# Performance work log

Measured on AMD Instinct MI355X. Metric: run time of the kernel, lower is better.

## Reference

```python
import jax, jax.numpy as jnp
import numpy as np

T = 1 << 20          # sequence length
THRESHOLD = 1e-4     # decay-reset threshold (module default)


def setup_inputs() -> dict:
    key = jax.random.key(0)
    X = jax.random.normal(key, (T,), dtype=jnp.float32)
    # stable params near module init [0.2, 0.2, 0.0, 0.0]; small w3/w4 keep the
    # quadratic recurrence bounded while exercising all terms.
    params = jnp.array([0.2, 0.2, 0.05, 0.01], dtype=jnp.float32)
    return {"X": X, "params": params}


def reference(X, params):
    dt = X.dtype
    w1 = jnp.tanh(params[0]); dtanh1 = 1.0 - w1 * w1; d2tanh1 = -2.0 * w1 * dtanh1
    w2 = jnp.tanh(params[1]); dtanh2 = 1.0 - w2 * w2; d2tanh2 = -2.0 * w2 * dtanh2
    w3, w4 = params[2], params[3]

    def step(carry, x):
        h, Jh, Hh, decay = carry  # h:(), Jh:(4,), Hh:(4,4), decay:()
        h_new = w1 * x + w2 * h + w3 * x * x + w4 * h * h
        df_dw = jnp.stack([x * dtanh1, h * dtanh2, x * x, h * h])
        df_dh = w2 + 2.0 * w4 * h
        Jh_new = df_dw + df_dh * Jh
        Hww = (jnp.zeros((4, 4), dt)
               .at[0, 0].set(x * d2tanh1)
               .at[1, 1].set(h * d2tanh2))
        g = jnp.zeros((4,), dt).at[1].set(dtanh2).at[3].set(2.0 * h)
        outer = g[:, None] * Jh[None, :]
        Hh_new = Hww + outer + outer.T + df_dh * Hh
        decay_new = decay * jnp.abs(df_dh)
        reset = decay_new < THRESHOLD
        # torch zero_() mutates storage in-place, so the appended J/H entries at a
        # reset step are also zeroed -> emit post-reset values.
        Jh_out = jnp.where(reset, jnp.zeros((4,), dt), Jh_new)
        Hh_out = jnp.where(reset, jnp.zeros((4, 4), dt), Hh_new)
        h_out = jnp.where(reset, jax.lax.stop_gradient(h_new), h_new)  # detach
        decay_out = jnp.where(reset, jnp.ones((), dt), decay_new)
        return (h_out, Jh_out, Hh_out, decay_out), (h_new, Jh_out, Hh_out)

    init = (jnp.zeros((), dt), jnp.zeros((4,), dt), jnp.zeros((4, 4), dt),
            jnp.ones((), dt))
    _, (hs, Js, Hs) = jax.lax.scan(step, init, X[:-1])
    Z = jnp.concatenate([jnp.zeros((1,), dt), hs])              # [T]
    J = jnp.concatenate([jnp.zeros((1, 4), dt), Js])            # [T, 4]
    H = jnp.concatenate([jnp.zeros((1, 4, 4), dt), Hs])         # [T, 4, 4]
    return Z, J, H
```

## Files before the change

kernel.cpp:

```cpp
#include <hip/hip_runtime.h>
#include <math.h>

#define TLEN (1 << 20)
#define SB 32
#define NSB (TLEN / SB)
#define SCB 256
#define NSCB (NSB / SCB)
#define THRESH 1e-4f
#define IDMAP 0x00FAC688u

#define WWORDS (SCB * SB + 8)
#define WPAD(i) ((i) + ((i) >> 5))
#define LDSW WPAD(WWORDS)

#pragma clang fp contract(off)


#define CHUNK55(OFS, OUTARR) {                                                 \
        const float4* xp_ = (const float4*)(X + (OFS) - 24);                   \
        float xa_[56];                                                         \
        _Pragma("unroll")                                                      \
        for (int q_ = 0; q_ < 14; ++q_) {                                      \
            float4 v_ = xp_[q_];                                               \
            xa_[4 * q_ + 0] = v_.x; xa_[4 * q_ + 1] = v_.y;                    \
            xa_[4 * q_ + 2] = v_.z; xa_[4 * q_ + 3] = v_.w;                    \
        }                                                                      \
        float h_ = 0.0f;                                                       \
        _Pragma("unroll")                                                      \
        for (int p_ = 0; p_ < 55; ++p_) {                                      \
            float x_ = xa_[p_];                                                \
            float t1_ = w1 * x_;                                               \
            float t2_ = w2 * h_;                                               \
            float s1_ = t1_ + t2_;                                             \
            float t3_ = (w3 * x_) * x_;                                        \
            float s2_ = s1_ + t3_;                                             \
            float t4_ = (w4 * h_) * h_;                                        \
            h_ = s2_ + t4_;                                                    \
            if (p_ >= 23) OUTARR[p_ - 23] = h_;                                \
        }                                                                      \
    }

__global__ void __launch_bounds__(256) k_zts(const float* __restrict__ P,
                                             const float* __restrict__ X,
                                             float* __restrict__ c,
                                             float* __restrict__ Z,
                                             unsigned int* __restrict__ L32,
                                             unsigned int* __restrict__ BT) {
#pragma clang fp contract(off)
    __shared__ float sc[4];
    __shared__ float zw[LDSW];
    __shared__ unsigned int buf[2][SCB];
    int t = threadIdx.x;
    int b = blockIdx.x;
    if (t == 0) {
        float tw1 = (float)tanh((double)P[0]);
        float tw2 = (float)tanh((double)P[1]);
        sc[0] = tw1; sc[1] = tw2; sc[2] = P[2]; sc[3] = P[3];
        if (b == 0) {
            float dt1 = 1.0f - tw1 * tw1;
            float dt2 = 1.0f - tw2 * tw2;
            c[0] = tw1; c[1] = tw2; c[2] = P[2]; c[3] = P[3];
            c[4] = dt1; c[5] = dt2;
            c[6] = (-2.0f * tw1) * dt1; c[7] = (-2.0f * tw2) * dt2;
            c[8] = 2.0f * P[3];
        }
    }
    __syncthreads();
    float w1 = sc[0], w2 = sc[1], w3 = sc[2], w4 = sc[3];
    float w42 = 2.0f * w4;
    long gi = (long)b * SCB + t;
    long o = gi * 32;
    float out[32];
    if (gi == 0) {
        float h = 0.0f;
        out[0] = 0.0f;
        for (int k = 0; k < 31; ++k) {
            float x = X[k];
            float t1 = w1 * x;
            float t2 = w2 * h;
            float s1 = t1 + t2;
            float t3 = (w3 * x) * x;
            float s2 = s1 + t3;
            float t4 = (w4 * h) * h;
            h = s2 + t4;
            out[k + 1] = h;
        }
    } else {
        CHUNK55(o, out);
    }
#pragma unroll
    for (int q = 0; q < 8; ++q)
        *(float4*)(Z + o + 4 * q) = make_float4(out[4 * q], out[4 * q + 1],
                                                out[4 * q + 2], out[4 * q + 3]);
    int rbase = t * 32 + 8;
#pragma unroll
    for (int k = 0; k < 32; ++k) zw[WPAD(rbase + k)] = out[k];
    if (t == 0 && b > 0) {
        long op = (long)b * (SCB * SB) - 32;
        float pout[32];
        CHUNK55(op, pout);
#pragma unroll
        for (int q = 0; q < 7; ++q) zw[WPAD(1 + q)] = pout[25 + q];
    }
    __syncthreads();
    unsigned int m32;
    if (gi < NSB - 1) {
        float d[8]; int last[8];
#pragma unroll
        for (int g = 0; g < 8; ++g) { d[g] = 1.0f; last[g] = -g; }
        if (gi == 0) {
#pragma unroll
            for (int g = 0; g < 8; ++g) last[g] = 0;
            for (int k = 0; k < 32; ++k) {
                float fa = fabsf(w2 + w42 * zw[WPAD(rbase + k)]);
#pragma unroll
                for (int g = 0; g < 8; ++g) {
                    d[g] = d[g] * fa;
                    if (d[g] < THRESH) { last[g] = k + 1; d[g] = 1.0f; }
                }
            }
        } else {
#pragma unroll
            for (int p = 0; p < 7; ++p) {
                float fa = fabsf(w2 + w42 * zw[WPAD(rbase + p - 7)]);
#pragma unroll
                for (int g = 7 - p; g < 8; ++g) {
                    d[g] = d[g] * fa;
                    if (d[g] < THRESH) { last[g] = p - 6; d[g] = 1.0f; }
                }
            }
            for (int k = 0; k < 32; ++k) {
                float fa = fabsf(w2 + w42 * zw[WPAD(rbase + k)]);
#pragma unroll
                for (int g = 0; g < 8; ++g) {
                    d[g] = d[g] * fa;
                    if (d[g] < THRESH) { last[g] = k + 1; d[g] = 1.0f; }
                }
            }
        }
        m32 = 0;
#pragma unroll
        for (int g = 0; g < 8; ++g) {
            int delta = 32 - last[g]; if (delta > 7) delta = 7;
            m32 |= (unsigned int)delta << (3 * g);
        }
    } else {
        m32 = IDMAP;
    }
    buf[0][t] = m32;
    __syncthreads();
    int cur = 0;
    for (int off = 1; off < SCB; off <<= 1) {
        unsigned int hi = buf[cur][t];
        unsigned int r;
        if (t >= off) {
            unsigned int lo = buf[cur][t - off];
            r = 0;
#pragma unroll
            for (int g = 0; g < 8; ++g) {
                unsigned int lg = (lo >> (3 * g)) & 7u;
                r |= ((hi >> (3 * lg)) & 7u) << (3 * g);
            }
        } else {
            r = hi;
        }
        buf[cur ^ 1][t] = r;
        __syncthreads();
        cur ^= 1;
    }
    L32[gi] = buf[cur][t];
    if (t == SCB - 1) BT[b] = buf[cur][t];
}

__global__ void __launch_bounds__(256) k_jh6(const float* __restrict__ X,
                                             const float* __restrict__ Z,
                                             const float* __restrict__ c,
                                             const unsigned int* __restrict__ L32,
                                             const unsigned int* __restrict__ BT,
                                             float* __restrict__ Jout,
                                             float* __restrict__ Hout) {
#pragma clang fp contract(off)
    __shared__ unsigned int sBT[NSCB];
    __shared__ unsigned char ages[256];
    __shared__ float zs[264];
    __shared__ float xs[264];
    __shared__ float hx[256 * 17];
    int t = threadIdx.x;
    int B = blockIdx.x;
    float w2 = c[1], dt1 = c[4], dt2 = c[5], d2t1 = c[6], d2t2 = c[7], w42 = c[8];
    long base = (long)B * 256 - 8;
    if (t < NSCB) sBT[t] = BT[t];
    if (t >= 128 && t < 194) {
        int s = t - 128;
        long zi = base + 4l * s;
        float4 v = make_float4(0.f, 0.f, 0.f, 0.f);
        if (zi >= 0) v = *(const float4*)(Z + zi);
        zs[4 * s] = v.x; zs[4 * s + 1] = v.y; zs[4 * s + 2] = v.z; zs[4 * s + 3] = v.w;
    } else if (t >= 194 && t < 260 - 0 && t < 256) {
        int s = t - 194;
        long zi = base + 4l * s;
        float4 v = make_float4(0.f, 0.f, 0.f, 0.f);
        if (zi >= 0) v = *(const float4*)(X + zi);
        xs[4 * s] = v.x; xs[4 * s + 1] = v.y; xs[4 * s + 2] = v.z; xs[4 * s + 3] = v.w;
    } else if (t >= 64 && t < 68) {
        int s = t - 64 + 62;
        long zi = base + 4l * s;
        float4 v = make_float4(0.f, 0.f, 0.f, 0.f);
        if (zi >= 0) v = *(const float4*)(X + zi);
        xs[4 * s] = v.x; xs[4 * s + 1] = v.y; xs[4 * s + 2] = v.z; xs[4 * s + 3] = v.w;
    }
    __syncthreads();
    if (t < 8) {
        int i = B * 8 + t;
        int e = 0;
        if (i > 0) {
            int bp = (i - 1) >> 8;
            unsigned int g = 0;
            for (int k = 0; k < bp; ++k) g = (sBT[k] >> (3 * g)) & 7u;
            e = (int)((L32[i - 1] >> (3 * g)) & 7u);
        }
        long ci = (long)i * SB;
        long r = ci - e;
        float d = 1.0f;
        long last = r;
        for (long m = r + 1; m <= ci; ++m) {
            float a = w2 + w42 * zs[(int)(m - 1 - base)];
            d = d * fabsf(a);
            if (d < THRESH) { last = m; d = 1.0f; }
        }
        ages[t * 32] = (unsigned char)(ci - last);
        for (int k = 1; k < SB; ++k) {
            long m = ci + k;
            float a = w2 + w42 * zs[(int)(m - 1 - base)];
            d = d * fabsf(a);
            if (d < THRESH) { last = m; d = 1.0f; }
            ages[t * 32 + k] = (unsigned char)(m - last);
        }
    }
    __syncthreads();
    long q = (long)B * 256 + t;
    int a = (int)ages[t];
    float J0 = 0, J1 = 0, J2 = 0, J3 = 0;
    float H00 = 0, H01 = 0, H03 = 0, H11 = 0, H12 = 0, H13 = 0, H23 = 0, H33 = 0;
    if (a > 0) {
        long m0 = q - a + 1;
        {
            int ix = (int)(m0 - 1 - base);
            float x = xs[ix];
            float h = zs[ix];
            H00 = x * d2t1; H11 = h * d2t2;
            J0 = x * dt1; J1 = h * dt2; J2 = x * x; J3 = h * h;
        }
        for (long m = m0 + 1; m <= q; ++m) {
            int ix = (int)(m - 1 - base);
            float x = xs[ix];
            float h = zs[ix];
            float av = w2 + w42 * h;
            float g3 = 2.0f * h;
            float g1J0 = dt2 * J0, g1J1 = dt2 * J1, g1J2 = dt2 * J2, g1J3 = dt2 * J3;
            float g3J0 = g3 * J0, g3J1 = g3 * J1, g3J2 = g3 * J2, g3J3 = g3 * J3;
            float n00 = (x * d2t1) + av * H00;
            float n01 = g1J0 + av * H01;
            float n03 = g3J0 + av * H03;
            float n11 = (((h * d2t2) + g1J1) + g1J1) + av * H11;
            float n12 = g1J2 + av * H12;
            float n13 = (g1J3 + g3J1) + av * H13;
            float n23 = g3J2 + av * H23;
            float n33 = (g3J3 + g3J3) + av * H33;
            H00 = n00; H01 = n01; H03 = n03; H11 = n11;
            H12 = n12; H13 = n13; H23 = n23; H33 = n33;
            J0 = (x * dt1) + av * J0;
            J1 = (h * dt2) + av * J1;
            J2 = (x * x) + av * J2;
            J3 = (h * h) + av * J3;
        }
    }
    *((float4*)(Jout + 4 * q)) = make_float4(J0, J1, J2, J3);
    float* hr = hx + t * 17;
    hr[0]  = H00; hr[1]  = H01; hr[2]  = 0.0f; hr[3]  = H03;
    hr[4]  = H01; hr[5]  = H11; hr[6]  = H12;  hr[7]  = H13;
    hr[8]  = 0.0f; hr[9] = H12; hr[10] = 0.0f; hr[11] = H23;
    hr[12] = H03; hr[13] = H13; hr[14] = H23;  hr[15] = H33;
    __syncthreads();
    float4* Hp = (float4*)Hout + (long)B * 1024;
#pragma unroll
    for (int rr = 0; rr < 4; ++rr) {
        int f = 256 * rr + t;
        int o = f >> 2;
        int cc = (f & 3) * 4;
        const float* s = hx + o * 17 + cc;
        Hp[f] = make_float4(s[0], s[1], s[2], s[3]);
    }
}

extern "C" void kernel_launch(void* const* d_in, const int* in_sizes, int n_in,
                              void* d_out, int out_size, void* d_ws, size_t ws_size,
                              hipStream_t stream) {
    const float* X = (const float*)d_in[0];
    const float* P = (const float*)d_in[1];
    float* out = (float*)d_out;
    float* Z = out;
    float* Jout = out + (long)TLEN;
    float* Hout = out + 5l * TLEN;

    char* ws = (char*)d_ws;
    float* consts = (float*)ws;
    unsigned int* BT = (unsigned int*)(ws + 64);
    unsigned int* L32 = (unsigned int*)(ws + 1024);

    hipLaunchKernelGGL(k_zts, dim3(NSCB), dim3(SCB), 0, stream,
                       P, X, consts, Z, L32, BT);
    hipLaunchKernelGGL(k_jh6, dim3(TLEN / 256), dim3(256), 0, stream,
                       X, Z, consts, L32, BT, Jout, Hout);
}
```

Before: 40.88 us.

## Precompute per-entry-age reset bitmasks in scan kernel, derive ages via clz

The first kernel now records, for each 32-step block and each of the 8 possible entry ages, a bitmask of positions where the decay resets, and writes these masks to workspace. The second kernel reads the masks and computes each thread's age since the last reset with a bit mask and count-leading-zeros. This replaces the serial 32-step decay replay that 8 threads ran per block while the other threads waited at a barrier. In exchange it adds 32 bytes per block of global writes and reads, plus mask bookkeeping inside the first kernel's decay loop.

```diff
diff --git a/kernel.cpp b/kernel.cpp
--- a/kernel.cpp
+++ b/kernel.cpp
@@ -45,7 +45,8 @@
                                              float* __restrict__ c,
                                              float* __restrict__ Z,
                                              unsigned int* __restrict__ L32,
-                                             unsigned int* __restrict__ BT) {
+                                             unsigned int* __restrict__ BT,
+                                             unsigned int* __restrict__ Msk) {
 #pragma clang fp contract(off)
     __shared__ float sc[4];
     __shared__ float zw[LDSW];
@@ -104,10 +105,11 @@
     }
     __syncthreads();
     unsigned int m32;
-    if (gi < NSB - 1) {
+    unsigned int msk[8];
+    {
         float d[8]; int last[8];
 #pragma unroll
-        for (int g = 0; g < 8; ++g) { d[g] = 1.0f; last[g] = -g; }
+        for (int g = 0; g < 8; ++g) { d[g] = 1.0f; last[g] = -g; msk[g] = 0u; }
         if (gi == 0) {
 #pragma unroll
             for (int g = 0; g < 8; ++g) last[g] = 0;
@@ -116,7 +118,7 @@
 #pragma unroll
                 for (int g = 0; g < 8; ++g) {
                     d[g] = d[g] * fa;
-                    if (d[g] < THRESH) { last[g] = k + 1; d[g] = 1.0f; }
+                    if (d[g] < THRESH) { last[g] = k + 1; d[g] = 1.0f; msk[g] |= 1u << k; }
                 }
             }
         } else {
@@ -134,19 +136,24 @@
 #pragma unroll
                 for (int g = 0; g < 8; ++g) {
                     d[g] = d[g] * fa;
-                    if (d[g] < THRESH) { last[g] = k + 1; d[g] = 1.0f; }
+                    if (d[g] < THRESH) { last[g] = k + 1; d[g] = 1.0f; msk[g] |= 1u << k; }
                 }
             }
         }
-        m32 = 0;
-#pragma unroll
-        for (int g = 0; g < 8; ++g) {
-            int delta = 32 - last[g]; if (delta > 7) delta = 7;
-            m32 |= (unsigned int)delta << (3 * g);
-        }
-    } else {
-        m32 = IDMAP;
-    }
+        if (gi < NSB - 1) {
+            m32 = 0;
+#pragma unroll
+            for (int g = 0; g < 8; ++g) {
+                int delta = 32 - last[g]; if (delta > 7) delta = 7;
+                m32 |= (unsigned int)delta << (3 * g);
+            }
+        } else {
+            m32 = IDMAP;
+        }
+    }
+    uint4* mp = (uint4*)Msk + gi * 2;
+    mp[0] = make_uint4(msk[0], msk[1], msk[2], msk[3]);
+    mp[1] = make_uint4(msk[4], msk[5], msk[6], msk[7]);
     buf[0][t] = m32;
     __syncthreads();
     int cur = 0;
@@ -172,16 +179,18 @@
     if (t == SCB - 1) BT[b] = buf[cur][t];
 }
 
-__global__ void __launch_bounds__(256) k_jh6(const float* __restrict__ X,
+__global__ void __launch_bounds__(256) k_jh7(const float* __restrict__ X,
                                              const float* __restrict__ Z,
                                              const float* __restrict__ c,
                                              const unsigned int* __restrict__ L32,
                                              const unsigned int* __restrict__ BT,
+                                             const unsigned int* __restrict__ Msk,
                                              float* __restrict__ Jout,
                                              float* __restrict__ Hout) {
 #pragma clang fp contract(off)
     __shared__ unsigned int sBT[NSCB];
-    __shared__ unsigned char ages[256];
+    __shared__ unsigned int smsk[64];
+    __shared__ unsigned char eL[8];
     __shared__ float zs[264];
     __shared__ float xs[264];
     __shared__ float hx[256 * 17];
@@ -190,13 +199,18 @@
     float w2 = c[1], dt1 = c[4], dt2 = c[5], d2t1 = c[6], d2t2 = c[7], w42 = c[8];
     long base = (long)B * 256 - 8;
     if (t < NSCB) sBT[t] = BT[t];
+    if (t < 16) {
+        uint4 v = ((const uint4*)Msk)[(long)B * 16 + t];
+        smsk[4 * t] = v.x; smsk[4 * t + 1] = v.y;
+        smsk[4 * t + 2] = v.z; smsk[4 * t + 3] = v.w;
+    }
     if (t >= 128 && t < 194) {
         int s = t - 128;
         long zi = base + 4l * s;
         float4 v = make_float4(0.f, 0.f, 0.f, 0.f);
         if (zi >= 0) v = *(const float4*)(Z + zi);
         zs[4 * s] = v.x; zs[4 * s + 1] = v.y; zs[4 * s + 2] = v.z; zs[4 * s + 3] = v.w;
-    } else if (t >= 194 && t < 260 - 0 && t < 256) {
+    } else if (t >= 194 && t < 256) {
         int s = t - 194;
         long zi = base + 4l * s;
         float4 v = make_float4(0.f, 0.f, 0.f, 0.f);
@@ -219,27 +233,17 @@
             for (int k = 0; k < bp; ++k) g = (sBT[k] >> (3 * g)) & 7u;
             e = (int)((L32[i - 1] >> (3 * g)) & 7u);
         }
-        long ci = (long)i * SB;
-        long r = ci - e;
-        float d = 1.0f;
-        long last = r;
-        for (long m = r + 1; m <= ci; ++m) {
-            float a = w2 + w42 * zs[(int)(m - 1 - base)];
-            d = d * fabsf(a);
-            if (d < THRESH) { last = m; d = 1.0f; }
-        }
-        ages[t * 32] = (unsigned char)(ci - last);
-        for (int k = 1; k < SB; ++k) {
-            long m = ci + k;
-            float a = w2 + w42 * zs[(int)(m - 1 - base)];
-            d = d * fabsf(a);
-            if (d < THRESH) { last = m; d = 1.0f; }
-            ages[t * 32 + k] = (unsigned char)(m - last);
-        }
+        eL[t] = (unsigned char)e;
     }
     __syncthreads();
     long q = (long)B * 256 + t;
-    int a = (int)ages[t];
+    int il = t >> 5;
+    int j = t & 31;
+    int e = (int)eL[il];
+    unsigned int mask = smsk[il * 8 + e];
+    unsigned int bits = mask & ((j > 0) ? ((1u << j) - 1u) : 0u);
+    int a = bits ? (j + __clz(bits) - 32) : (j + e);
+
     float J0 = 0, J1 = 0, J2 = 0, J3 = 0;
     float H00 = 0, H01 = 0, H03 = 0, H11 = 0, H12 = 0, H13 = 0, H23 = 0, H33 = 0;
     if (a > 0) {
@@ -307,9 +311,10 @@
     float* consts = (float*)ws;
     unsigned int* BT = (unsigned int*)(ws + 64);
     unsigned int* L32 = (unsigned int*)(ws + 1024);
+    unsigned int* Msk = (unsigned int*)(ws + 1024 + (size_t)NSB * 4);
 
     hipLaunchKernelGGL(k_zts, dim3(NSCB), dim3(SCB), 0, stream,
-                       P, X, consts, Z, L32, BT);
-    hipLaunchKernelGGL(k_jh6, dim3(TLEN / 256), dim3(256), 0, stream,
-                       X, Z, consts, L32, BT, Jout, Hout);
+                       P, X, consts, Z, L32, BT, Msk);
+    hipLaunchKernelGGL(k_jh7, dim3(TLEN / 256), dim3(256), 0, stream,
+                       X, Z, consts, L32, BT, Msk, Jout, Hout);
 }
```

After: 40.73 us. Within noise of the previous version (-0.4%).
